# Kernel tuning notes

Hardware: AMD Instinct MI355X
Metric: run time of the kernel (lower is better)

Reference implementation:

```python
import jax, jax.numpy as jnp
import numpy as np

POOL = 7
IMG_DIM = 1024.0
NUM_CLASSES = 81
EPS = 1e-3


def crop_and_resize(fmap, boxes, P):
    """TF-style crop_and_resize with extrapolation_value=0.
    fmap: [C,H,W] (all box_indices are 0 in the original), boxes: [R,4] normalized (y1,x1,y2,x2).
    Returns [R,C,P,P]."""
    C, H, W = fmap.shape
    y1, x1, y2, x2 = boxes[:, 0], boxes[:, 1], boxes[:, 2], boxes[:, 3]
    g = jnp.arange(P, dtype=fmap.dtype) / (P - 1)  # [P]
    ys = y1[:, None] * (H - 1) + g[None, :] * ((y2 - y1) * (H - 1))[:, None]  # [R,P]
    xs = x1[:, None] * (W - 1) + g[None, :] * ((x2 - x1) * (W - 1))[:, None]  # [R,P]

    def axis(coords, size):
        valid = (coords >= 0) & (coords <= size - 1)
        c = jnp.clip(coords, 0, size - 1)
        lo = jnp.floor(c)
        hi = jnp.minimum(lo + 1, size - 1)
        return lo.astype(jnp.int32), hi.astype(jnp.int32), c - lo, valid

    y_lo, y_hi, wy, vy = axis(ys, H)
    x_lo, x_hi, wx, vx = axis(xs, W)

    def gather(yi, xi):  # -> [C,R,P,P]
        return fmap[:, yi[:, :, None], xi[:, None, :]]

    wxe = wx[None, :, None, :]
    top = gather(y_lo, x_lo) * (1 - wxe) + gather(y_lo, x_hi) * wxe
    bot = gather(y_hi, x_lo) * (1 - wxe) + gather(y_hi, x_hi) * wxe
    wye = wy[None, :, :, None]
    out = top * (1 - wye) + bot * wye
    mask = (vy[:, :, None] & vx[:, None, :])[None]  # [1,R,P,P]
    out = jnp.where(mask, out, jnp.zeros((), fmap.dtype))
    return jnp.transpose(out, (1, 0, 2, 3))  # [R,C,P,P]


def roi_align(fmaps, rois_flat):
    """rois_flat: [R,4] pixel coords (x1,y1,x2,y2). fmaps: list of 4 [C,H,W] (levels 2..5)."""
    x1, y1, x2, y2 = rois_flat[:, 0], rois_flat[:, 1], rois_flat[:, 2], rois_flat[:, 3]
    s = jnp.sqrt(jnp.maximum((y2 - y1) * (x2 - x1), 0.0))
    roi_level = jnp.log(s / 224.0) / np.log(2.0)
    roi_level = jnp.clip(jnp.round(roi_level) + 4, 2, 5)  # [R]
    boxes_norm = (rois_flat / IMG_DIM)[:, [1, 0, 3, 2]]  # (y1,x1,y2,x2)
    pooled = jnp.zeros((rois_flat.shape[0], fmaps[0].shape[0], POOL, POOL), rois_flat.dtype)
    for i, level in enumerate(range(2, 6)):
        crops = crop_and_resize(fmaps[i], boxes_norm, POOL)  # [R,C,P,P]
        sel = (roi_level == level)[:, None, None, None]
        pooled = jnp.where(sel, crops, pooled)
    return pooled  # [R,C,P,P]


def bn(x, g, b, m, v):  # inference batchnorm over channel axis (last)
    return (x - m) * (g / jnp.sqrt(v + EPS)) + b


def head(pooled, conv1_w, conv1_b, bn1_g, bn1_b, bn1_m, bn1_v,
         conv2_w, conv2_b, bn2_g, bn2_b, bn2_m, bn2_v,
         logits_w, logits_b, bbox_w, bbox_b):
    # conv1: 7x7 'valid' conv collapsing spatial dims -> dense [R,1024]
    x = jnp.einsum('rchw,kchw->rk', pooled, conv1_w) + conv1_b
    x = jax.nn.relu(bn(x, bn1_g, bn1_b, bn1_m, bn1_v))
    x = x @ conv2_w.T + conv2_b  # 1x1 conv == matmul
    shared = jax.nn.relu(bn(x, bn2_g, bn2_b, bn2_m, bn2_v))
    logits = shared @ logits_w.T + logits_b          # [R,NC]
    probs = jax.nn.softmax(logits, axis=-1)
    bbox = (shared @ bbox_w.T + bbox_b).reshape(-1, NUM_CLASSES, 4)
    return logits, probs, bbox


def setup_inputs() -> dict:
    key = jax.random.key(0)
    ks = jax.random.split(key, 24)
    B, N, C = 1, 1000, 256
    d = {}
    sizes = [256, 128, 64, 32]
    for i, s in enumerate(sizes):
        d[f'p{i+2}'] = jax.random.normal(ks[i], (B, C, s, s), jnp.float32)
    # valid boxes in pixel coords (x1,y1,x2,y2) spanning all pyramid levels
    cx = jax.random.uniform(ks[4], (B, N), minval=100.0, maxval=924.0)
    cy = jax.random.uniform(ks[5], (B, N), minval=100.0, maxval=924.0)
    hw = jax.random.uniform(ks[6], (B, N), minval=8.0, maxval=400.0)
    hh = jax.random.uniform(ks[7], (B, N), minval=8.0, maxval=400.0)
    rois = jnp.stack([jnp.clip(cx - hw, 0, 1024), jnp.clip(cy - hh, 0, 1024),
                      jnp.clip(cx + hw, 0, 1024), jnp.clip(cy + hh, 0, 1024)], axis=-1)
    d['rois'] = rois.astype(jnp.float32)
    sc = 0.02
    d['conv1_w'] = jax.random.normal(ks[8], (1024, 256, POOL, POOL)) * sc
    d['conv1_b'] = jnp.zeros((1024,), jnp.float32)
    d['bn1_g'] = jnp.ones((1024,), jnp.float32)
    d['bn1_b'] = jnp.zeros((1024,), jnp.float32)
    d['bn1_m'] = jnp.zeros((1024,), jnp.float32)
    d['bn1_v'] = jnp.ones((1024,), jnp.float32)
    d['conv2_w'] = jax.random.normal(ks[9], (1024, 1024)) * sc
    d['conv2_b'] = jnp.zeros((1024,), jnp.float32)
    d['bn2_g'] = jnp.ones((1024,), jnp.float32)
    d['bn2_b'] = jnp.zeros((1024,), jnp.float32)
    d['bn2_m'] = jnp.zeros((1024,), jnp.float32)
    d['bn2_v'] = jnp.ones((1024,), jnp.float32)
    d['logits_w'] = jax.random.normal(ks[10], (NUM_CLASSES, 1024)) * sc
    d['logits_b'] = jnp.zeros((NUM_CLASSES,), jnp.float32)
    d['bbox_w'] = jax.random.normal(ks[11], (NUM_CLASSES * 4, 1024)) * sc
    d['bbox_b'] = jnp.zeros((NUM_CLASSES * 4,), jnp.float32)
    return d


def reference(p2, p3, p4, p5, rois,
              conv1_w, conv1_b, bn1_g, bn1_b, bn1_m, bn1_v,
              conv2_w, conv2_b, bn2_g, bn2_b, bn2_m, bn2_v,
              logits_w, logits_b, bbox_w, bbox_b):
    B, N = rois.shape[0], rois.shape[1]
    fmaps = [p2[0], p3[0], p4[0], p5[0]]  # box_indices are all 0 in the original
    rois_flat = rois.reshape(B * N, 4)
    pooled = roi_align(fmaps, rois_flat)  # [B*N,256,7,7]
    logits, probs, bbox = head(pooled, conv1_w, conv1_b, bn1_g, bn1_b, bn1_m, bn1_v,
                               conv2_w, conv2_b, bn2_g, bn2_b, bn2_m, bn2_v,
                               logits_w, logits_b, bbox_w, bbox_b)
    return (logits.reshape(B, N, NUM_CLASSES),
            probs.reshape(B, N, NUM_CLASSES),
            bbox.reshape(B, N, NUM_CLASSES, 4))
```

## Files before the change

### kernel.cpp

```cpp
#include <hip/hip_runtime.h>
#include <hip/hip_fp16.h>
#include <math.h>

typedef _Float16 f16;
typedef _Float16 half8 __attribute__((ext_vector_type(8)));
typedef _Float16 half4v __attribute__((ext_vector_type(4)));
typedef _Float16 half2v __attribute__((ext_vector_type(2)));
typedef float f32x4 __attribute__((ext_vector_type(4)));


__device__ __forceinline__ void gload16(const f16* g, f16* lds) {
  __builtin_amdgcn_global_load_lds(
      (const __attribute__((address_space(1))) unsigned int*)g,
      (__attribute__((address_space(3))) unsigned int*)lds, 16, 0, 0);
}

__device__ __forceinline__ void fmap_body(int b, f16* tile,
                                          const float* __restrict__ p2,
                                          const float* __restrict__ p3,
                                          const float* __restrict__ p4,
                                          const float* __restrict__ p5,
                                          f16* __restrict__ dst0) {
  const float* src;
  int Ppix, p0;
  size_t dstoff;
  if (b < 512)      { src = p2; Ppix = 65536; dstoff = 0;     p0 = b * 128; }
  else if (b < 640) { src = p3; Ppix = 16384; dstoff = 65536; p0 = (b - 512) * 128; }
  else if (b < 672) { src = p4; Ppix = 4096;  dstoff = 81920; p0 = (b - 640) * 128; }
  else              { src = p5; Ppix = 1024;  dstoff = 86016; p0 = (b - 672) * 128; }
  const int t = threadIdx.x;
  const int px4 = (t & 31) * 4;
  const int cp = (t >> 5) * 2;
#pragma unroll 4
  for (int i = 0; i < 16; i++) {
    const int c = i * 16 + cp;
    const float4 va = *(const float4*)&src[(size_t)c * Ppix + p0 + px4];
    const float4 vb = *(const float4*)&src[(size_t)(c + 1) * Ppix + p0 + px4];
    const float a_[4] = {va.x, va.y, va.z, va.w};
    const float b_[4] = {vb.x, vb.y, vb.z, vb.w};
#pragma unroll
    for (int j = 0; j < 4; j++) {
      const int px = px4 + j;
      const int cs = c ^ (((px >> 2) & 31) << 3);
      half2v h = {(f16)a_[j], (f16)b_[j]};
      *(half2v*)&tile[px * 256 + cs] = h;
    }
  }
  __syncthreads();
  f16* d = dst0 + (dstoff + (size_t)p0) * 256;
  const int c8 = (t & 31) * 8;
#pragma unroll 4
  for (int i = 0; i < 16; i++) {
    const int px = (t >> 5) * 16 + i;
    const int c8s = c8 ^ (((px >> 2) & 31) << 3);
    const half8 o = *(const half8*)&tile[px * 256 + c8s];
    *(half8*)&d[px * 256 + c8] = o;
  }
}

__device__ __forceinline__ void w1t_body(int k, f16* tile,
                                         const float* __restrict__ w1,
                                         f16* __restrict__ w1t) {
  const int t = threadIdx.x;
  const float* src = w1 + (size_t)k * 12544;
  f16* dst = w1t + (size_t)k * 12544;
#pragma unroll 7
  for (int i = 0; i < 49; i++) {
    const int idx = i * 256 + t;
    const int c = idx / 49, pq = idx % 49;
    tile[pq * 260 + c] = (f16)src[idx];
  }
  __syncthreads();
#pragma unroll
  for (int i = 0; i < 7; i++) {
    const int h8 = i * 256 + t;
    if (h8 < 1568) {
      const int pq = h8 >> 5, c8 = (h8 & 31) * 8;
      const half4v lo = *(const half4v*)&tile[pq * 260 + c8];
      const half4v hi = *(const half4v*)&tile[pq * 260 + c8 + 4];
      half8 o;
      o[0] = lo[0]; o[1] = lo[1]; o[2] = lo[2]; o[3] = lo[3];
      o[4] = hi[0]; o[5] = hi[1]; o[6] = hi[2]; o[7] = hi[3];
      *(half8*)&dst[pq * 256 + c8] = o;
    }
  }
}

__global__ __launch_bounds__(256) void prep_big_k(const float* __restrict__ p2,
                                                  const float* __restrict__ p3,
                                                  const float* __restrict__ p4,
                                                  const float* __restrict__ p5,
                                                  const float* __restrict__ conv1_w,
                                                  f16* __restrict__ fmapT,
                                                  f16* __restrict__ w1t) {
  __shared__ __align__(16) f16 buf[32768];
  const int bid = blockIdx.x;
  const int g = bid / 5, r = bid % 5;
  if (r < 2) {
    const int fb = g * 2 + r;
    if (fb < 680) fmap_body(fb, buf, p2, p3, p4, p5, fmapT);
  } else {
    const int wb = g * 3 + (r - 2);
    if (wb < 1024) w1t_body(wb, buf, conv1_w, w1t);
  }
}

__global__ void prep_small_k(const float* __restrict__ conv2_w,
                             const float* __restrict__ lw, const float* __restrict__ lb,
                             const float* __restrict__ bw, const float* __restrict__ bb,
                             f16* __restrict__ w2t, f16* __restrict__ wcat,
                             float* __restrict__ bcat) {
  const int i = blockIdx.x * 256 + threadIdx.x;
  if (i < 262144) {
    const float4 v = ((const float4*)conv2_w)[i];
    half4v o = {(f16)v.x, (f16)v.y, (f16)v.z, (f16)v.w};
    ((half4v*)w2t)[i] = o;
  } else if (i < 262144 + 131072) {
    const int idx4 = i - 262144;
    const int elem = idx4 * 4;
    const int row = elem >> 10, col = elem & 1023;
    half4v o;
#pragma unroll
    for (int j = 0; j < 4; j++) {
      float v = 0.f;
      if (row < 81) v = lw[row * 1024 + col + j];
      else if (row < 405) v = bw[(row - 81) * 1024 + col + j];
      o[j] = (f16)v;
    }
    ((half4v*)wcat)[idx4] = o;
  } else if (i < 262144 + 131072 + 128) {
    const int j = (i - 393216) * 4;
    float r[4];
#pragma unroll
    for (int q = 0; q < 4; q++) {
      const int c = j + q;
      float bv = 0.f;
      if (c < 81) bv = lb[c];
      else if (c < 405) bv = bb[c - 81];
      r[q] = bv;
    }
    float4 o;
    o.x = r[0]; o.y = r[1]; o.z = r[2]; o.w = r[3];
    *(float4*)&bcat[j] = o;
  }
}

__global__ __launch_bounds__(256) void roi_align_k(const float* __restrict__ rois,
                                                   const f16* __restrict__ fmapT,
                                                   f16* __restrict__ pooled) {
  const int t = threadIdx.x;
  const int hf = t >> 7, tp = t & 127;
  const int r = blockIdx.x * 2 + hf;
  __shared__ int s_lo[2][14], s_hi[2][14], s_val[2][14];
  __shared__ float s_w[2][14];
  const bool live = (r < 1000);
  int H = 2, off = 0;
  if (live) {
    const float x1 = rois[r * 4 + 0], y1 = rois[r * 4 + 1];
    const float x2 = rois[r * 4 + 2], y2 = rois[r * 4 + 3];
    const float s = sqrtf(fmaxf((y2 - y1) * (x2 - x1), 0.f));
    const float lf = logf(s / 224.0f) / 0.69314718055994531f;
    int lv = (int)rintf(lf) + 4;
    lv = lv < 2 ? 2 : (lv > 5 ? 5 : lv);
    const int li = lv - 2;
    H = 256 >> li;
    off = (li == 0) ? 0 : (li == 1) ? 65536 : (li == 2) ? 81920 : 86016;
    const float Hm1 = (float)(H - 1);
    if (tp < 14) {
      const bool isx = tp >= 7;
      const int i = isx ? tp - 7 : tp;
      const float b1 = (isx ? x1 : y1) * (1.0f / 1024.0f);
      const float b2 = (isx ? x2 : y2) * (1.0f / 1024.0f);
      const float g = (float)i / 6.0f;
      const float coord = b1 * Hm1 + g * ((b2 - b1) * Hm1);
      const int valid = (coord >= 0.f) && (coord <= Hm1);
      float c = fminf(fmaxf(coord, 0.f), Hm1);
      float lo = floorf(c);
      s_lo[hf][tp] = (int)lo;
      s_hi[hf][tp] = (int)fminf(lo + 1.f, Hm1);
      s_w[hf][tp] = c - lo;
      s_val[hf][tp] = valid;
    }
  }
  __syncthreads();
  f16* outp = pooled + (size_t)r * 12544 + 2 * tp;
  if (!live) {
#pragma unroll 7
    for (int i = 0; i < 49; i++) {
      half2v z = {(f16)0.f, (f16)0.f};
      *(half2v*)&outp[i * 256] = z;
    }
    return;
  }
  const f16* base = fmapT + (size_t)off * 256 + 2 * tp;
  for (int py = 0; py < 7; py++) {
    const int ylo = s_lo[hf][py], yhi = s_hi[hf][py], vy = s_val[hf][py];
    const float wy = s_w[hf][py];
    for (int px = 0; px < 7; px++) {
      const int xlo = s_lo[hf][7 + px], xhi = s_hi[hf][7 + px], vx = s_val[hf][7 + px];
      const float wx = s_w[hf][7 + px];
      const half2v v00 = *(const half2v*)&base[(size_t)(ylo * H + xlo) * 256];
      const half2v v01 = *(const half2v*)&base[(size_t)(ylo * H + xhi) * 256];
      const half2v v10 = *(const half2v*)&base[(size_t)(yhi * H + xlo) * 256];
      const half2v v11 = *(const half2v*)&base[(size_t)(yhi * H + xhi) * 256];
      half2v o;
#pragma unroll
      for (int q = 0; q < 2; q++) {
        const float top = (float)v00[q] * (1.f - wx) + (float)v01[q] * wx;
        const float bot = (float)v10[q] * (1.f - wx) + (float)v11[q] * wx;
        float vv = top * (1.f - wy) + bot * wy;
        if (!(vy && vx)) vv = 0.f;
        o[q] = (f16)vv;
      }
      *(half2v*)&outp[(py * 7 + px) * 256] = o;
    }
  }
}

__global__ __launch_bounds__(512) void gemm1_d2(
    const f16* __restrict__ A, const f16* __restrict__ B, float* __restrict__ part,
    int K, int kPerSplit) {
  __shared__ __align__(16) f16 As[4][256 * 32];
  __shared__ __align__(16) f16 Bs[4][128 * 32];
  const int t = threadIdx.x;

  int lid = blockIdx.x + 8 * (blockIdx.y + 4 * blockIdx.z);
  const int chunk = (8 * 4 * (int)gridDim.z) >> 3;
  lid = (lid & 7) * chunk + (lid >> 3);
  const int bx = lid & 7;
  const int by = (lid >> 3) & 3;
  const int bz = lid >> 5;

  const int m0 = by * 256, n0 = bx * 128;
  const int wid = t >> 6, lane = t & 63;
  const int wr = (wid & 3) * 64;
  const int wc = (wid >> 2) * 64;
  const int lrow = lane & 15;
  const int lsl = lane >> 4;
  const int srow = t >> 2;
  const int scol = (((t & 3) ^ ((t >> 3) & 3)) << 3);
  const int kz0 = bz * kPerSplit;
  const int nIter = kPerSplit >> 5;

  f32x4 acc[4][4] = {};
  const f16* Ab = A + (size_t)(m0 + srow) * K + kz0 + scol;
  const f16* Bb = B + (size_t)(n0 + srow) * K + kz0 + scol;
  f16* asb = &As[0][0] + wid * 512;
  f16* bsb = &Bs[0][0] + wid * 512;

#define STG(kt) do {                                                           \
    const int sl_ = (kt) & 3; const size_t ko_ = (size_t)(kt) * 32;            \
    gload16(Ab + ko_, asb + sl_ * 8192);                                       \
    gload16(Ab + (size_t)128 * K + ko_, asb + sl_ * 8192 + 4096);              \
    gload16(Bb + ko_, bsb + sl_ * 4096);                                       \
    __builtin_amdgcn_sched_barrier(0);                                         \
  } while (0)

  STG(0);
  STG(1);
  asm volatile("s_waitcnt vmcnt(3)" ::: "memory");
  __builtin_amdgcn_sched_barrier(0);
  __builtin_amdgcn_s_barrier();

  for (int kt = 0; kt < nIter; ++kt) {
    const int sl = kt & 3;
    const f16* as = &As[sl][0];
    const f16* bs = &Bs[sl][0];
    half8 aF[4], bF[4];
#pragma unroll
    for (int m = 0; m < 4; m++) {
      const int r_ = wr + m * 16 + lrow;
      aF[m] = *(const half8*)&as[r_ * 32 + ((lsl ^ ((r_ >> 1) & 3)) << 3)];
    }
#pragma unroll
    for (int n = 0; n < 4; n++) {
      const int r_ = wc + n * 16 + lrow;
      bF[n] = *(const half8*)&bs[r_ * 32 + ((lsl ^ ((r_ >> 1) & 3)) << 3)];
    }
    if (kt + 2 < nIter) STG(kt + 2);
    __builtin_amdgcn_s_setprio(1);
#pragma unroll
    for (int m = 0; m < 4; m++)
#pragma unroll
      for (int n = 0; n < 4; n++)
        acc[m][n] = __builtin_amdgcn_mfma_f32_16x16x32_f16(aF[m], bF[n], acc[m][n], 0, 0, 0);
    __builtin_amdgcn_s_setprio(0);
    if (kt + 2 < nIter) { asm volatile("s_waitcnt vmcnt(3)" ::: "memory"); }
    else                { asm volatile("s_waitcnt vmcnt(0)" ::: "memory"); }
    __builtin_amdgcn_sched_barrier(0);
    __builtin_amdgcn_s_barrier();
  }
#undef STG

  float* outp = part + (size_t)bz * (1024 * 1024);
#pragma unroll
  for (int m = 0; m < 4; m++) {
    const int rr = m0 + wr + m * 16 + lsl * 4;
#pragma unroll
    for (int n = 0; n < 4; n++) {
      const int cc = n0 + wc + n * 16 + lrow;
#pragma unroll
      for (int j = 0; j < 4; j++)
        outp[(size_t)(rr + j) * 1024 + cc] = acc[m][n][j];
    }
  }
}

__global__ __launch_bounds__(256) void gemm_nt_p3(
    const f16* __restrict__ A, const f16* __restrict__ B, float* __restrict__ part,
    int K, int kPerSplit, int ldc) {
  __shared__ __align__(16) f16 As[3][128 * 32];
  __shared__ __align__(16) f16 Bs[3][128 * 32];
  const int t = threadIdx.x;

  const int gx = gridDim.x, gy = gridDim.y;
  int lid = blockIdx.x + gx * (blockIdx.y + gy * blockIdx.z);
  const int chunk = (gx * gy * (int)gridDim.z) >> 3;
  lid = (lid & 7) * chunk + (lid >> 3);
  const int bx = lid % gx;
  const int tmp = lid / gx;
  const int by = tmp % gy;
  const int bz = tmp / gy;

  const int m0 = by * 128;
  const int n0 = bx * 128;
  const int wid = t >> 6;
  const int lane = t & 63;
  const int wr = (wid >> 1) * 64;
  const int wc = (wid & 1) * 64;
  const int lrow = lane & 15;
  const int lsl = lane >> 4;
  const int rowA = t >> 2;
  const int c8 = (((t & 3) ^ ((rowA >> 1) & 3)) << 3);
  const int kz0 = bz * kPerSplit;
  const int nIter = kPerSplit >> 5;

  f32x4 acc[4][4] = {};
  const f16* Ab = A + (size_t)m0 * K + kz0 + c8;
  const f16* Bb = B + (size_t)n0 * K + kz0 + c8;

#define STAGE(buf, it)                                                        \
  do {                                                                        \
    const int ko = (it) * 32;                                                 \
    gload16(Ab + (size_t)rowA * K + ko, &As[buf][wid * 512]);                 \
    gload16(Ab + (size_t)(rowA + 64) * K + ko, &As[buf][2048 + wid * 512]);   \
    gload16(Bb + (size_t)rowA * K + ko, &Bs[buf][wid * 512]);                 \
    gload16(Bb + (size_t)(rowA + 64) * K + ko, &Bs[buf][2048 + wid * 512]);   \
  } while (0)

#define COMPUTE(buf)                                                          \
  do {                                                                        \
    half8 aF[4], bF[4];                                                       \
    _Pragma("unroll") for (int m = 0; m < 4; m++) {                           \
      const int rr_ = wr + m * 16 + lrow;                                     \
      aF[m] = *(const half8*)&As[buf][rr_ * 32 + ((lsl ^ ((rr_ >> 1) & 3)) << 3)]; \
    }                                                                         \
    _Pragma("unroll") for (int n = 0; n < 4; n++) {                           \
      const int rr_ = wc + n * 16 + lrow;                                     \
      bF[n] = *(const half8*)&Bs[buf][rr_ * 32 + ((lsl ^ ((rr_ >> 1) & 3)) << 3)]; \
    }                                                                         \
    __builtin_amdgcn_s_setprio(1);                                            \
    _Pragma("unroll") for (int m = 0; m < 4; m++)                             \
      _Pragma("unroll") for (int n = 0; n < 4; n++)                           \
        acc[m][n] = __builtin_amdgcn_mfma_f32_16x16x32_f16(aF[m], bF[n], acc[m][n], 0, 0, 0); \
    __builtin_amdgcn_s_setprio(0);                                            \
  } while (0)

  STAGE(0, 0);
  STAGE(1, 1);
  int bc = 0;
  for (int it = 0; it < nIter - 2; ++it) {
    const int bs_ = (bc == 0) ? 2 : bc - 1;
    STAGE(bs_, it + 2);
    asm volatile("s_waitcnt vmcnt(8)" ::: "memory");
    __builtin_amdgcn_sched_barrier(0);
    __builtin_amdgcn_s_barrier();
    COMPUTE(bc);
    __builtin_amdgcn_s_barrier();
    bc = (bc == 2) ? 0 : bc + 1;
  }
  asm volatile("s_waitcnt vmcnt(4)" ::: "memory");
  __builtin_amdgcn_sched_barrier(0);
  __builtin_amdgcn_s_barrier();
  COMPUTE(bc);
  __builtin_amdgcn_s_barrier();
  bc = (bc == 2) ? 0 : bc + 1;
  asm volatile("s_waitcnt vmcnt(0)" ::: "memory");
  __builtin_amdgcn_sched_barrier(0);
  __builtin_amdgcn_s_barrier();
  COMPUTE(bc);
#undef STAGE
#undef COMPUTE

  const size_t slice = (size_t)gy * 128 * ldc;
#pragma unroll
  for (int m = 0; m < 4; m++) {
#pragma unroll
    for (int n = 0; n < 4; n++) {
#pragma unroll
      for (int j = 0; j < 4; j++) {
        const int rr = m0 + wr + m * 16 + ((lane >> 4) << 2) + j;
        const int cc = n0 + wc + n * 16 + (lane & 15);
        part[(size_t)bz * slice + (size_t)rr * ldc + cc] = acc[m][n][j];
      }
    }
  }
}

template <int Z>
__global__ void reduce_ep_k(const float* __restrict__ part, int sliceE, int ldc,
                            const float* __restrict__ bias, const float* __restrict__ g,
                            const float* __restrict__ b, const float* __restrict__ m,
                            const float* __restrict__ v, f16* __restrict__ out) {
  const int i4 = (blockIdx.x * 256 + threadIdx.x) * 4;
  float4 s = *(const float4*)(part + i4);
#pragma unroll
  for (int z = 1; z < Z; z++) {
    const float4 p = *(const float4*)(part + (size_t)z * sliceE + i4);
    s.x += p.x; s.y += p.y; s.z += p.z; s.w += p.w;
  }
  const int c0 = i4 % ldc;
  float r[4] = {s.x, s.y, s.z, s.w};
  half4v o;
#pragma unroll
  for (int j = 0; j < 4; j++) {
    const int c = c0 + j;
    const float x = r[j] + bias[c];
    const float sc = g[c] / sqrtf(v[c] + 1e-3f);
    o[j] = (f16)fmaxf((x - m[c]) * sc + b[c], 0.f);
  }
  *(half4v*)(out + i4) = o;
}

__global__ __launch_bounds__(256) void reduce3_out_k(const float* __restrict__ part,
                                                     const float* __restrict__ bcat,
                                                     float* __restrict__ out) {
  const int r = blockIdx.x, t = threadIdx.x;
  __shared__ float red[256];
  const float* base = part + (size_t)r * 512;
  float v0 = 0.f, v1 = 0.f;
  {
    float s = bcat[t];
#pragma unroll
    for (int z = 0; z < 8; z++) s += base[(size_t)z * 524288 + t];
    v0 = s;
  }
  if (t < 149) {
    float s = bcat[256 + t];
#pragma unroll
    for (int z = 0; z < 8; z++) s += base[(size_t)z * 524288 + 256 + t];
    v1 = s;
  }
  red[t] = (t < 81) ? v0 : -INFINITY;
  __syncthreads();
  for (int s_ = 128; s_ > 0; s_ >>= 1) {
    if (t < s_) red[t] = fmaxf(red[t], red[t + s_]);
    __syncthreads();
  }
  const float mx = red[0];
  __syncthreads();
  const float e = (t < 81) ? expf(v0 - mx) : 0.f;
  red[t] = e;
  __syncthreads();
  for (int s_ = 128; s_ > 0; s_ >>= 1) {
    if (t < s_) red[t] += red[t + s_];
    __syncthreads();
  }
  const float inv = 1.f / red[0];
  if (t < 81) {
    out[(size_t)r * 81 + t] = v0;
    out[81000 + (size_t)r * 81 + t] = e * inv;
  }
  if (t >= 81) out[162000 + (size_t)r * 324 + (t - 81)] = v0;
  if (t < 149) out[162000 + (size_t)r * 324 + 175 + t] = v1;
}

extern "C" void kernel_launch(void* const* d_in, const int* in_sizes, int n_in,
                              void* d_out, int out_size, void* d_ws, size_t ws_size,
                              hipStream_t stream) {
  const float* p2 = (const float*)d_in[0];
  const float* p3 = (const float*)d_in[1];
  const float* p4 = (const float*)d_in[2];
  const float* p5 = (const float*)d_in[3];
  const float* rois = (const float*)d_in[4];
  const float* conv1_w = (const float*)d_in[5];
  const float* conv1_b = (const float*)d_in[6];
  const float* bn1_g = (const float*)d_in[7];
  const float* bn1_b = (const float*)d_in[8];
  const float* bn1_m = (const float*)d_in[9];
  const float* bn1_v = (const float*)d_in[10];
  const float* conv2_w = (const float*)d_in[11];
  const float* conv2_b = (const float*)d_in[12];
  const float* bn2_g = (const float*)d_in[13];
  const float* bn2_b = (const float*)d_in[14];
  const float* bn2_m = (const float*)d_in[15];
  const float* bn2_v = (const float*)d_in[16];
  const float* logits_w = (const float*)d_in[17];
  const float* logits_b = (const float*)d_in[18];
  const float* bbox_w = (const float*)d_in[19];
  const float* bbox_b = (const float*)d_in[20];

  char* ws = (char*)d_ws;
  f16* fmapT = (f16*)ws;
  f16* sh1 = (f16*)(ws + (size_t)0);
  f16* sh2 = (f16*)(ws + ((size_t)2 << 20));
  f16* w2t = (f16*)(ws + ((size_t)6 << 20));
  f16* wcat = (f16*)(ws + ((size_t)8 << 20));
  float* bcat = (float*)(ws + ((size_t)9 << 20));
  float* part = (float*)(ws + ((size_t)10 << 20));
  f16* pooled = (f16*)(ws + (size_t)44564480);
  f16* w1t = (f16*)(ws + (size_t)70254592);

  prep_big_k<<<1710, 256, 0, stream>>>(p2, p3, p4, p5, conv1_w, fmapT, w1t);
  roi_align_k<<<512, 256, 0, stream>>>(rois, fmapT, pooled);
  prep_small_k<<<1537, 256, 0, stream>>>(conv2_w, logits_w, logits_b, bbox_w, bbox_b,
                                         w2t, wcat, bcat);
  gemm1_d2<<<dim3(8, 4, 8), 512, 0, stream>>>(pooled, w1t, part, 12544, 1568);
  reduce_ep_k<8><<<1024, 256, 0, stream>>>(part, 1048576, 1024, conv1_b, bn1_g,
                                           bn1_b, bn1_m, bn1_v, sh1);
  gemm_nt_p3<<<dim3(8, 8, 4), 256, 0, stream>>>(sh1, w2t, part, 1024, 256, 1024);
  reduce_ep_k<4><<<1024, 256, 0, stream>>>(part, 1048576, 1024, conv2_b, bn2_g,
                                           bn2_b, bn2_m, bn2_v, sh2);
  gemm_nt_p3<<<dim3(4, 8, 8), 256, 0, stream>>>(sh2, wcat, part, 1024, 128, 512);
  reduce3_out_k<<<1000, 256, 0, stream>>>(part, bcat, (float*)d_out);
}
```

Measured before the change: 124.0 us.

## Skip P2 transpose; sample level-2 features directly from fp32 NCHW in ROI align

The P2 feature map (256x256x256 fp32) is no longer transposed and converted to fp16 channels-last in the prep kernel. ROIs assigned to level 2 now gather bilinear samples straight from the original fp32 NCHW tensor. Only the three smaller levels are still transposed. This removes the largest pass of reads and writes in prep. In exchange, the level-2 gathers are scalar fp32 loads with a large channel stride and poor coalescing. The fmapT buffer moves and launch order changes so prep_small runs first.

Result: slower. 172.6 us (+39.2%).

```diff
diff --git a/kernel.cpp b/kernel.cpp
--- a/kernel.cpp
+++ b/kernel.cpp
@@ -16,7 +16,6 @@
 }
 
 __device__ __forceinline__ void fmap_body(int b, f16* tile,
-                                          const float* __restrict__ p2,
                                           const float* __restrict__ p3,
                                           const float* __restrict__ p4,
                                           const float* __restrict__ p5,
@@ -24,10 +23,9 @@
   const float* src;
   int Ppix, p0;
   size_t dstoff;
-  if (b < 512)      { src = p2; Ppix = 65536; dstoff = 0;     p0 = b * 128; }
-  else if (b < 640) { src = p3; Ppix = 16384; dstoff = 65536; p0 = (b - 512) * 128; }
-  else if (b < 672) { src = p4; Ppix = 4096;  dstoff = 81920; p0 = (b - 640) * 128; }
-  else              { src = p5; Ppix = 1024;  dstoff = 86016; p0 = (b - 672) * 128; }
+  if (b < 128)      { src = p3; Ppix = 16384; dstoff = 0;     p0 = b * 128; }
+  else if (b < 160) { src = p4; Ppix = 4096;  dstoff = 16384; p0 = (b - 128) * 128; }
+  else              { src = p5; Ppix = 1024;  dstoff = 20480; p0 = (b - 160) * 128; }
   const int t = threadIdx.x;
   const int px4 = (t & 31) * 4;
   const int cp = (t >> 5) * 2;
@@ -86,8 +84,7 @@
   }
 }
 
-__global__ __launch_bounds__(256) void prep_big_k(const float* __restrict__ p2,
-                                                  const float* __restrict__ p3,
+__global__ __launch_bounds__(256) void prep_big_k(const float* __restrict__ p3,
                                                   const float* __restrict__ p4,
                                                   const float* __restrict__ p5,
                                                   const float* __restrict__ conv1_w,
@@ -95,12 +92,11 @@
                                                   f16* __restrict__ w1t) {
   __shared__ __align__(16) f16 buf[32768];
   const int bid = blockIdx.x;
-  const int g = bid / 5, r = bid % 5;
-  if (r < 2) {
-    const int fb = g * 2 + r;
-    if (fb < 680) fmap_body(fb, buf, p2, p3, p4, p5, fmapT);
+  const int g = bid / 7, r = bid % 7;
+  if (r == 0) {
+    if (g < 168) fmap_body(g, buf, p3, p4, p5, fmapT);
   } else {
-    const int wb = g * 3 + (r - 2);
+    const int wb = g * 6 + (r - 1);
     if (wb < 1024) w1t_body(wb, buf, conv1_w, w1t);
   }
 }
@@ -146,6 +142,7 @@
 }
 
 __global__ __launch_bounds__(256) void roi_align_k(const float* __restrict__ rois,
+                                                   const float* __restrict__ p2,
                                                    const f16* __restrict__ fmapT,
                                                    f16* __restrict__ pooled) {
   const int t = threadIdx.x;
@@ -154,7 +151,7 @@
   __shared__ int s_lo[2][14], s_hi[2][14], s_val[2][14];
   __shared__ float s_w[2][14];
   const bool live = (r < 1000);
-  int H = 2, off = 0;
+  int li = 0, H = 2, off = 0;
   if (live) {
     const float x1 = rois[r * 4 + 0], y1 = rois[r * 4 + 1];
     const float x2 = rois[r * 4 + 2], y2 = rois[r * 4 + 3];
@@ -162,9 +159,9 @@
     const float lf = logf(s / 224.0f) / 0.69314718055994531f;
     int lv = (int)rintf(lf) + 4;
     lv = lv < 2 ? 2 : (lv > 5 ? 5 : lv);
-    const int li = lv - 2;
+    li = lv - 2;
     H = 256 >> li;
-    off = (li == 0) ? 0 : (li == 1) ? 65536 : (li == 2) ? 81920 : 86016;
+    off = (li == 1) ? 0 : (li == 2) ? 16384 : 20480;
     const float Hm1 = (float)(H - 1);
     if (tp < 14) {
       const bool isx = tp >= 7;
@@ -183,8 +180,8 @@
     }
   }
   __syncthreads();
-  f16* outp = pooled + (size_t)r * 12544 + 2 * tp;
   if (!live) {
+    f16* outp = pooled + (size_t)r * 12544 + 2 * tp;
 #pragma unroll 7
     for (int i = 0; i < 49; i++) {
       half2v z = {(f16)0.f, (f16)0.f};
@@ -192,6 +189,39 @@
     }
     return;
   }
+  if (li == 0) {
+    f16* outp = pooled + (size_t)r * 12544;
+    const size_t cstr = 65536;
+    const float* b0 = p2 + (size_t)tp * cstr;
+    const float* b1 = p2 + (size_t)(tp + 128) * cstr;
+    for (int py = 0; py < 7; py++) {
+      const int ylo = s_lo[hf][py], yhi = s_hi[hf][py], vy = s_val[hf][py];
+      const float wy = s_w[hf][py];
+#pragma unroll
+      for (int px = 0; px < 7; px++) {
+        const int xlo = s_lo[hf][7 + px], xhi = s_hi[hf][7 + px], vx = s_val[hf][7 + px];
+        const float wx = s_w[hf][7 + px];
+        const int o00 = ylo * 256 + xlo, o01 = ylo * 256 + xhi;
+        const int o10 = yhi * 256 + xlo, o11 = yhi * 256 + xhi;
+        float res[2];
+#pragma unroll
+        for (int q = 0; q < 2; q++) {
+          const float* bb_ = q ? b1 : b0;
+          const float v00 = bb_[o00], v01 = bb_[o01];
+          const float v10 = bb_[o10], v11 = bb_[o11];
+          const float top = v00 * (1.f - wx) + v01 * wx;
+          const float bot = v10 * (1.f - wx) + v11 * wx;
+          float vv = top * (1.f - wy) + bot * wy;
+          if (!(vy && vx)) vv = 0.f;
+          res[q] = vv;
+        }
+        outp[(py * 7 + px) * 256 + tp] = (f16)res[0];
+        outp[(py * 7 + px) * 256 + tp + 128] = (f16)res[1];
+      }
+    }
+    return;
+  }
+  f16* outp = pooled + (size_t)r * 12544 + 2 * tp;
   const f16* base = fmapT + (size_t)off * 256 + 2 * tp;
   for (int py = 0; py < 7; py++) {
     const int ylo = s_lo[hf][py], yhi = s_hi[hf][py], vy = s_val[hf][py];
@@ -501,20 +531,20 @@
   const float* bbox_b = (const float*)d_in[20];
 
   char* ws = (char*)d_ws;
-  f16* fmapT = (f16*)ws;
   f16* sh1 = (f16*)(ws + (size_t)0);
   f16* sh2 = (f16*)(ws + ((size_t)2 << 20));
   f16* w2t = (f16*)(ws + ((size_t)6 << 20));
   f16* wcat = (f16*)(ws + ((size_t)8 << 20));
   float* bcat = (float*)(ws + ((size_t)9 << 20));
+  f16* fmapT = (f16*)(ws + (size_t)9961472);
   float* part = (float*)(ws + ((size_t)10 << 20));
   f16* pooled = (f16*)(ws + (size_t)44564480);
   f16* w1t = (f16*)(ws + (size_t)70254592);
 
-  prep_big_k<<<1710, 256, 0, stream>>>(p2, p3, p4, p5, conv1_w, fmapT, w1t);
-  roi_align_k<<<512, 256, 0, stream>>>(rois, fmapT, pooled);
   prep_small_k<<<1537, 256, 0, stream>>>(conv2_w, logits_w, logits_b, bbox_w, bbox_b,
                                          w2t, wcat, bcat);
+  prep_big_k<<<1197, 256, 0, stream>>>(p3, p4, p5, conv1_w, fmapT, w1t);
+  roi_align_k<<<512, 256, 0, stream>>>(rois, p2, fmapT, pooled);
   gemm1_d2<<<dim3(8, 4, 8), 512, 0, stream>>>(pooled, w1t, part, 12544, 1568);
   reduce_ep_k<8><<<1024, 256, 0, stream>>>(part, 1048576, 1024, conv1_b, bn1_g,
                                            bn1_b, bn1_m, bn1_v, sh1);
```
